# Performance work log

Hardware: AMD Instinct MI355X
Metric: run time of the kernel (lower is better)

The kernel has to match this reference:

```python
import jax, jax.numpy as jnp
import numpy as np

L, H, Z, B, SRC, K = 2, 1024, 256, 128, 64, 48
IN = Z + 1 + H  # z_i (+) k (+) attn


def _init(key, shape, fan_in):
    return jax.random.normal(key, shape, jnp.float32) / np.sqrt(fan_in)


def setup_inputs() -> dict:
    key = jax.random.key(0)
    ks = jax.random.split(key, 24)
    inp = {
        "h0": jax.random.normal(ks[0], (L, B, H), jnp.float32),
        "c0": jax.random.normal(ks[1], (L, B, H), jnp.float32),
        "context": jax.random.normal(ks[2], (B, SRC, H), jnp.float32),
        "z_0": jax.random.normal(ks[3], (B, Z), jnp.float32),
        "k": jax.random.randint(ks[4], (B, 1), 1, K + 1, jnp.int32),
        "eps": jax.random.normal(ks[5], (K, B, Z), jnp.float32),
        # StackedLSTM layer 0 (input IN) and layer 1 (input H)
        "W_ih0": _init(ks[6], (4 * H, IN), IN), "W_hh0": _init(ks[7], (4 * H, H), H),
        "b_ih0": jnp.zeros((4 * H,), jnp.float32), "b_hh0": jnp.zeros((4 * H,), jnp.float32),
        "W_ih1": _init(ks[8], (4 * H, H), H), "W_hh1": _init(ks[9], (4 * H, H), H),
        "b_ih1": jnp.zeros((4 * H,), jnp.float32), "b_hh1": jnp.zeros((4 * H,), jnp.float32),
        # GlobalAttentionLatent (Luong general)
        "attn_W_in": _init(ks[10], (H, H), H), "attn_W_out": _init(ks[11], (H, 2 * H), 2 * H),
        # GeneratorLatent
        "mu_W": _init(ks[12], (Z, H), H), "mu_b": jnp.zeros((Z,), jnp.float32),
        "sigma_W": _init(ks[13], (Z, H), H), "sigma_b": jnp.zeros((Z,), jnp.float32),
    }
    return inp


def _lstm_cell(x, h, c, W_ih, W_hh, b_ih, b_hh):
    gates = x @ W_ih.T + b_ih + h @ W_hh.T + b_hh
    i, f, g, o = jnp.split(gates, 4, axis=1)
    c_new = jax.nn.sigmoid(f) * c + jax.nn.sigmoid(i) * jnp.tanh(g)
    h_new = jax.nn.sigmoid(o) * jnp.tanh(c_new)
    return h_new, c_new


def _attend(q, context, W_in, W_out):
    # q: [B,H], context: [B,S,H] -> [B,H]
    scores = jnp.einsum('bsh,bh->bs', context, q @ W_in.T)
    align = jax.nn.softmax(scores, axis=1)
    weighted = jnp.einsum('bs,bsh->bh', align, context)
    return jnp.tanh(jnp.concatenate([weighted, q], axis=1) @ W_out.T)


def _forward(h0, c0, context, z_0, k, eps,
             W_ih0, W_hh0, b_ih0, b_hh0, W_ih1, W_hh1, b_ih1, b_hh1,
             attn_W_in, attn_W_out, mu_W, mu_b, sigma_W, sigma_b):
    k_max = eps.shape[0]
    k_f = k.astype(jnp.float32)  # [B,1]
    attn0 = _attend(c0[-1], context, attn_W_in, attn_W_out)

    def step(carry, inp):
        z_i, attn_o, h, c = carry
        i, eps_i = inp
        x = jnp.concatenate([z_i, k_f, attn_o], axis=1)  # [B, Z+1+H]
        h0n, c0n = _lstm_cell(x, h[0], c[0], W_ih0, W_hh0, b_ih0, b_hh0)
        h1n, c1n = _lstm_cell(h0n, h[1], c[1], W_ih1, W_hh1, b_ih1, b_hh1)
        h_new = jnp.stack([h0n, h1n])
        c_new = jnp.stack([c0n, c1n])
        frozen = (i >= k_f).astype(h_new.dtype)[None]  # [1,B,1]
        h_new = frozen * h + (1.0 - frozen) * h_new
        c_new = frozen * c + (1.0 - frozen) * c_new
        output = h1n  # rnn output before freezing, as in torch
        mu_i = output @ mu_W.T + mu_b
        sig_i = output @ sigma_W.T + sigma_b
        z_next = mu_i + jnp.exp(sig_i) * eps_i
        attn_new = _attend(output, context, attn_W_in, attn_W_out)
        return (z_next, attn_new, h_new, c_new), (z_next, mu_i, sig_i)

    steps = jnp.arange(k_max, dtype=jnp.float32)
    (_, _, h_f, c_f), (z, mu, sigma) = jax.lax.scan(
        step, (z_0, attn0, h0, c0), (steps, eps))
    valid = (steps[:, None] < k_f[:, 0][None, :])[:, :, None]  # [K,B,1]
    z = jnp.where(valid, z, 0.0)
    mu = jnp.where(valid, mu, 0.0)
    sigma = jnp.where(valid, sigma, 0.0)
    return (z.transpose(1, 0, 2), mu.transpose(1, 0, 2), sigma.transpose(1, 0, 2), h_f, c_f)


def reference(h0, c0, context, z_0, k, eps,
              W_ih0, W_hh0, b_ih0, b_hh0, W_ih1, W_hh1, b_ih1, b_hh1,
              attn_W_in, attn_W_out, mu_W, mu_b, sigma_W, sigma_b):
    return _forward(h0, c0, context, z_0, k, eps,
                    W_ih0, W_hh0, b_ih0, b_hh0, W_ih1, W_hh1, b_ih1, b_hh1,
                    attn_W_in, attn_W_out, mu_W, mu_b, sigma_W, sigma_b)
```

## Files before the change

kernel.cpp:

```cpp
#include <hip/hip_runtime.h>
#include <hip/hip_bf16.h>

#define L_ 2
#define H_ 1024
#define Z_ 256
#define B_ 128
#define SRC_ 64
#define K_ 48
#define BH_ (B_ * H_)
#define BZ_ (B_ * Z_)
#define BKZ_ ((size_t)B_ * K_ * Z_)
#define KA_ 2304
#define KB_ 2048

typedef unsigned short u16;
typedef __attribute__((ext_vector_type(8))) short short8;
typedef __attribute__((ext_vector_type(4))) float f32x4;

__device__ __align__(16) u16 g_Wc0[4096 * KA_];
__device__ __align__(16) u16 g_Wc1[4096 * KB_];
__device__ __align__(16) u16 g_Wmq[512 * 1024];
__device__ __align__(16) u16 g_Woutb[1024 * 2048];
__device__ __align__(16) u16 g_WinT[1024 * 1024];
__device__ __align__(16) u16 g_ctxb[8192 * 1024];
__device__ __align__(16) u16 g_ctxW[8192 * 1024];
__device__ __align__(16) u16 g_ctxWin[8192 * 1024];
__device__ __align__(16) u16 g_XA[2][B_ * KA_];
__device__ __align__(16) u16 g_XB[2][B_ * KB_];
__device__ __align__(16) u16 g_XC[B_ * H_];
__device__ float g_pb0[4096], g_pb1[4096], g_pbmq[512], g_wk0[4096];
__device__ float g_cs0[BH_], g_cs1[BH_], g_align[B_ * SRC_];
__device__ float g_cred[B_ * H_];
__device__ int g_perm[B_], g_inv[B_], g_kr[B_], g_Mact[K_];

__device__ __forceinline__ float sigm(float x) { return 1.0f / (1.0f + expf(-x)); }
__device__ __forceinline__ u16 f2b(float f) {
    union { float f; unsigned u; } x; x.f = f;
    unsigned r = x.u + 0x7fffu + ((x.u >> 16) & 1u);
    return (u16)(r >> 16);
}
__device__ __forceinline__ float b2f(u16 s) {
    union { unsigned u; float f; } x; x.u = ((unsigned)s) << 16;
    return x.f;
}

#define PREPALL_NBLK_ 22017
__global__ __launch_bounds__(256) void k_prepall(
        const float* __restrict__ Wih0, const float* __restrict__ Whh0,
        const float* __restrict__ bih0, const float* __restrict__ bhh0,
        const float* __restrict__ Wih1, const float* __restrict__ Whh1,
        const float* __restrict__ bih1, const float* __restrict__ bhh1,
        const float* __restrict__ muW, const float* __restrict__ mub,
        const float* __restrict__ sgW, const float* __restrict__ sgb,
        const float* __restrict__ Win, const float* __restrict__ Wout,
        const float* __restrict__ ctx, const int* __restrict__ kvec,
        float* __restrict__ out) {
    __shared__ float shf[32 * 33];
    const int bid = blockIdx.x, tid = threadIdx.x;
    if (bid < 4096) {
        int n = bid, h = n >> 2, g = n & 3, r = g * 1024 + h;
        u16* row = g_Wc0 + (size_t)n * KA_;
        for (int j = tid; j < KA_; j += 256) {
            float v = (j < 256) ? Wih0[(size_t)r * 1281 + j]
                    : (j < 1280) ? Wih0[(size_t)r * 1281 + j + 1]
                                 : Whh0[(size_t)r * 1024 + (j - 1280)];
            row[j] = f2b(v);
        }
        if (tid == 0) {
            g_wk0[n] = Wih0[(size_t)r * 1281 + 256];
            g_pb0[n] = bih0[r] + bhh0[r];
        }
    } else if (bid < 8192) {
        int n = bid - 4096, h = n >> 2, g = n & 3, r = g * 1024 + h;
        u16* row = g_Wc1 + (size_t)n * KB_;
        for (int j = tid; j < KB_; j += 256) {
            float v = (j < 1024) ? Wih1[(size_t)r * 1024 + j]
                                 : Whh1[(size_t)r * 1024 + (j - 1024)];
            row[j] = f2b(v);
        }
        if (tid == 0) g_pb1[n] = bih1[r] + bhh1[r];
    } else if (bid < 8704) {
        int n = bid - 8192, z = n >> 1, sel = n & 1;
        const float* src = sel ? sgW : muW;
        u16* row = g_Wmq + (size_t)n * 1024;
        for (int j = tid; j < 1024; j += 256) row[j] = f2b(src[(size_t)z * 1024 + j]);
        if (tid == 0) g_pbmq[n] = sel ? sgb[z] : mub[z];
    } else if (bid < 9728) {
        int loc = bid - 8704;
        int bx = (loc & 31) * 32, by = (loc >> 5) * 32;
        int tx = tid & 31, ty0 = tid >> 5;
        for (int it = 0; it < 4; ++it) {
            int ty = ty0 + it * 8;
            shf[ty * 33 + tx] = Win[(size_t)(by + ty) * 1024 + bx + tx];
        }
        __syncthreads();
        for (int it = 0; it < 4; ++it) {
            int ty = ty0 + it * 8;
            g_WinT[(size_t)(bx + ty) * 1024 + by + tx] = f2b(shf[tx * 33 + ty]);
        }
    } else if (bid == 9728) {
        int* ks = (int*)shf;
        if (tid < B_) ks[tid] = kvec[tid];
        __syncthreads();
        if (tid < B_) {
            int kb = ks[tid], rank = 0;
            for (int j = 0; j < B_; ++j) {
                int kj = ks[j];
                rank += (kj > kb) || (kj == kb && j < tid);
            }
            g_perm[rank] = tid; g_inv[tid] = rank; g_kr[rank] = kb;
        }
        if (tid < K_) {
            int c = 0;
            for (int j = 0; j < B_; ++j) c += (ks[j] > tid);
            g_Mact[tid] = c;
        }
    } else if (bid < 11777) {
        int loc = bid - 9729;
        const int n = 1024 * 2048;
        for (int i = loc * 256 + tid; i < n; i += 2048 * 256)
            g_Woutb[i] = f2b(Wout[i]);
    } else if (bid < 19969) {
        int loc = bid - 11777;
        const int n = 8192 * 1024;
        for (int i = loc * 256 + tid; i < n; i += 8192 * 256)
            g_ctxb[i] = f2b(ctx[i]);
    } else {
        int loc = bid - 19969;
        size_t n = 3 * BKZ_;
        for (size_t i = (size_t)loc * 256 + tid; i < n; i += (size_t)2048 * 256)
            out[i] = 0.f;
    }
}

template <int K>
__device__ __forceinline__ void mmq(const u16* __restrict__ A, int sA,
                                    const u16* __restrict__ W, int sW,
                                    int m0, int n0, int w, int lane, f32x4& acc) {
    constexpr int KQ = K / 4;
    const int quad = lane >> 4, l16 = lane & 15;
    const u16* pa = A + (size_t)(m0 + l16) * sA + w * KQ + quad * 8;
    const u16* pw = W + (size_t)(n0 + l16) * sW + w * KQ + quad * 8;
#pragma unroll 4
    for (int k0 = 0; k0 < KQ; k0 += 32) {
        short8 a = *(const short8*)(const void*)(pa + k0);
        short8 b = *(const short8*)(const void*)(pw + k0);
        acc = __builtin_amdgcn_mfma_f32_16x16x32_bf16(a, b, acc, 0, 0, 0);
    }
}

__device__ __forceinline__ void stage_q(float* sm, int w, int lane, const f32x4& acc) {
    int quad = lane >> 4, l16 = lane & 15;
#pragma unroll
    for (int r = 0; r < 4; ++r) sm[w * 272 + (quad * 4 + r) * 17 + l16] = acc[r];
}

template <int K>
__device__ __forceinline__ void mm32(const u16* __restrict__ A, int sA,
                                     const u16* __restrict__ W, int sW,
                                     int m0, int n0, int w, int lane, f32x4 acc[2][2]) {
    constexpr int KQ = K / 4;
    const int quad = lane >> 4, l16 = lane & 15;
    const u16* pa0 = A + (size_t)(m0 + l16) * sA + w * KQ + quad * 8;
    const u16* pa1 = pa0 + (size_t)16 * sA;
    const u16* pb0 = W + (size_t)(n0 + l16) * sW + w * KQ + quad * 8;
    const u16* pb1 = pb0 + (size_t)16 * sW;
#pragma unroll 4
    for (int k0 = 0; k0 < KQ; k0 += 32) {
        short8 a0 = *(const short8*)(const void*)(pa0 + k0);
        short8 a1 = *(const short8*)(const void*)(pa1 + k0);
        short8 b0 = *(const short8*)(const void*)(pb0 + k0);
        short8 b1 = *(const short8*)(const void*)(pb1 + k0);
        acc[0][0] = __builtin_amdgcn_mfma_f32_16x16x32_bf16(a0, b0, acc[0][0], 0, 0, 0);
        acc[0][1] = __builtin_amdgcn_mfma_f32_16x16x32_bf16(a0, b1, acc[0][1], 0, 0, 0);
        acc[1][0] = __builtin_amdgcn_mfma_f32_16x16x32_bf16(a1, b0, acc[1][0], 0, 0, 0);
        acc[1][1] = __builtin_amdgcn_mfma_f32_16x16x32_bf16(a1, b1, acc[1][1], 0, 0, 0);
    }
}

template <int LAYER>
__global__ __launch_bounds__(256) void k_lstm(int step) {
    constexpr int K = (LAYER == 0) ? KA_ : KB_;
    const int p = step & 1;
    const u16* A = (LAYER == 0) ? g_XA[p] : g_XB[p];
    const u16* W = (LAYER == 0) ? g_Wc0 : g_Wc1;
    const float* pb = (LAYER == 0) ? g_pb0 : g_pb1;
    float* cs = (LAYER == 0) ? g_cs0 : g_cs1;
    const u16* stOld = (LAYER == 0) ? (g_XA[p] + 1280) : (g_XB[p] + 1024);
    u16* stNew = (LAYER == 0) ? (g_XA[1 - p] + 1280) : (g_XB[1 - p] + 1024);
    u16* hout = (LAYER == 0) ? g_XB[p] : g_XC;
    const int hoStride = (LAYER == 0) ? KB_ : 1024;

    const int tid = threadIdx.x, w = tid >> 6, lane = tid & 63;
    const int xcd = blockIdx.x & 7, loc = blockIdx.x >> 3;
    const int mt = loc & 3, nl = loc >> 2;
    const int m0 = mt * 32;
    const int n0 = (xcd * 16 + nl) * 32;
    const int Mact = g_Mact[step];

    if (m0 >= Mact) {
        const int r = m0 + (tid & 31), hg = (n0 >> 2) + (tid >> 5);
        stNew[(size_t)r * K + hg] = stOld[(size_t)r * K + hg];
        return;
    }

    __shared__ float smf[4 * 32 * 33];
    f32x4 acc[2][2] = {};
    mm32<K>(A, K, W, K, m0, n0, w, lane, acc);
    const int quad = lane >> 4, l16 = lane & 15;
#pragma unroll
    for (int i = 0; i < 2; ++i)
#pragma unroll
        for (int j = 0; j < 2; ++j)
#pragma unroll
            for (int r = 0; r < 4; ++r)
                smf[(w * 32 + i * 16 + quad * 4 + r) * 33 + j * 16 + l16] = acc[i][j][r];
    __syncthreads();
    const int bl = tid & 31, hl = tid >> 5;
    const int r = m0 + bl;
    float g[4];
#pragma unroll
    for (int gg = 0; gg < 4; ++gg) {
        int c = hl * 4 + gg;
        float s = smf[bl * 33 + c] + smf[(32 + bl) * 33 + c] +
                  smf[(64 + bl) * 33 + c] + smf[(96 + bl) * 33 + c];
        g[gg] = s + pb[n0 + c];
    }
    const int kr = g_kr[r];
    if (LAYER == 0) {
        float kf = (float)kr;
#pragma unroll
        for (int gg = 0; gg < 4; ++gg) g[gg] += kf * g_wk0[n0 + hl * 4 + gg];
    }
    const int hg = (n0 >> 2) + hl;
    float cold = cs[r * 1024 + hg];
    float cn = sigm(g[1]) * cold + sigm(g[0]) * tanhf(g[2]);
    float hn = sigm(g[3]) * tanhf(cn);
    hout[(size_t)r * hoStride + hg] = f2b(hn);
    if (step < kr) {
        stNew[(size_t)r * K + hg] = f2b(hn);
        cs[r * 1024 + hg] = cn;
    } else {
        stNew[(size_t)r * K + hg] = stOld[(size_t)r * K + hg];
    }
}

__global__ __launch_bounds__(256) void k_mix(const float* __restrict__ eps,
                                             float* __restrict__ out, int step,
                                             int do_mu, int do_sc) {
    __shared__ float sm[1344];
    const int tid = threadIdx.x;
    const int Mact = g_Mact[step];
    if (blockIdx.x < 256) {
        if (!do_mu) return;
        const int w = tid >> 6, lane = tid & 63;
        const int xcd = blockIdx.x & 7, loc = blockIdx.x >> 3;
        const int mt = loc & 7, nl = loc >> 3;
        const int m0 = mt * 16;
        const int n0 = (xcd * 4 + nl) * 16;
        if (m0 >= Mact) return;
        f32x4 acc = {0.f, 0.f, 0.f, 0.f};
        mmq<1024>(g_XC, 1024, g_Wmq, 1024, m0, n0, w, lane, acc);
        stage_q(sm, w, lane, acc);
        __syncthreads();
        if (tid < 128) {
            int bl = tid & 15, zl = tid >> 4;
            int r = m0 + bl;
            int c0 = 2 * zl, c1 = 2 * zl + 1;
            float mu = sm[bl * 17 + c0] + sm[272 + bl * 17 + c0] +
                       sm[544 + bl * 17 + c0] + sm[816 + bl * 17 + c0] + g_pbmq[n0 + c0];
            float sg = sm[bl * 17 + c1] + sm[272 + bl * 17 + c1] +
                       sm[544 + bl * 17 + c1] + sm[816 + bl * 17 + c1] + g_pbmq[n0 + c1];
            int zg = (n0 >> 1) + zl;
            int b = g_perm[r];
            float e = eps[((size_t)step * B_ + b) * Z_ + zg];
            float zn = mu + expf(sg) * e;
            g_XA[(step + 1) & 1][(size_t)r * KA_ + zg] = f2b(zn);
            bool valid = step < g_kr[r];
            size_t o = ((size_t)b * K_ + step) * Z_ + zg;
            out[o] = valid ? zn : 0.f;
            out[BKZ_ + o] = valid ? mu : 0.f;
            out[2 * BKZ_ + o] = valid ? sg : 0.f;
        }
    } else if (blockIdx.x < 384) {
        if (!do_sc) return;
        const int r = blockIdx.x - 256;
        if (r >= Mact) return;
        float* qf = sm;
        float* parts = sm + 1024;
        for (int i = tid; i < 1024; i += 256) qf[i] = b2f(g_XC[r * 1024 + i]);
        __syncthreads();
        int s = tid >> 2, part = tid & 3;
        const int b = g_perm[r];
        const u16* row = g_ctxWin + ((size_t)(b * SRC_ + s)) * 1024 + part * 256;
        float pacc = 0.f;
        for (int j = 0; j < 256; j += 8) {
            short8 v = *(const short8*)(const void*)(row + j);
#pragma unroll
            for (int t = 0; t < 8; ++t) pacc += qf[part * 256 + j + t] * b2f(((u16*)&v)[t]);
        }
        parts[s * 4 + part] = pacc;
        __syncthreads();
        if (tid < 64) {
            float v = parts[tid * 4] + parts[tid * 4 + 1] + parts[tid * 4 + 2] + parts[tid * 4 + 3];
            float mx = v;
            for (int o = 32; o; o >>= 1) mx = fmaxf(mx, __shfl_xor(mx, o, 64));
            float e = expf(v - mx), sum = e;
            for (int o = 32; o; o >>= 1) sum += __shfl_xor(sum, o, 64);
            g_align[r * SRC_ + tid] = e / sum;
        }
    } else {
        if (!do_sc) return;
        const int w = tid >> 6, lane = tid & 63;
        const int t = blockIdx.x - 384;
        const int xcd = t & 7, loc = t >> 3;
        const int mt = loc & 7, nl = loc >> 3;
        const int m0 = mt * 16;
        const int n0 = (xcd * 8 + nl) * 16;
        if (m0 >= Mact) return;
        f32x4 acc = {0.f, 0.f, 0.f, 0.f};
        mmq<1024>(g_XC, 1024, g_Woutb + 1024, 2048, m0, n0, w, lane, acc);
        stage_q(sm, w, lane, acc);
        __syncthreads();
        int bl = tid >> 4, hc = tid & 15;
        float cred = sm[bl * 17 + hc] + sm[272 + bl * 17 + hc] +
                     sm[544 + bl * 17 + hc] + sm[816 + bl * 17 + hc];
        g_cred[(size_t)(m0 + bl) * 1024 + n0 + hc] = cred;
    }
}

__global__ __launch_bounds__(256) void k_contract(int dp, int step) {
    __shared__ float sm[16 * SRC_];
    const int tid = threadIdx.x;
    const int xcd = blockIdx.x & 7, loc = blockIdx.x >> 3;
    const int mt = loc & 7, nl = loc >> 3;
    const int m0 = mt * 16;
    const int n0 = (xcd * 8 + nl) * 16;
    if (m0 >= g_Mact[step]) return;
    for (int i = tid; i < 16 * SRC_; i += 256)
        sm[i] = g_align[(m0 + (i >> 6)) * SRC_ + (i & 63)];
    __syncthreads();
    int bl = tid >> 4, hc = tid & 15;
    int r = m0 + bl;
    const int b = g_perm[r];
    const u16* base = g_ctxW + ((size_t)b * SRC_) * 1024 + n0 + hc;
    float a = g_cred[(size_t)r * 1024 + n0 + hc];
#pragma unroll 8
    for (int s = 0; s < SRC_; ++s) a += sm[bl * 64 + s] * b2f(base[(size_t)s * 1024]);
    g_XA[dp][(size_t)r * KA_ + 256 + n0 + hc] = f2b(tanhf(a));
}

__global__ __launch_bounds__(256) void k_gemminit(const float* __restrict__ h0,
                                                  const float* __restrict__ c0,
                                                  const float* __restrict__ z0) {
    const int bid = blockIdx.x, tid = threadIdx.x;
    if (bid < 2048) {
        const int sel = bid & 1;
        const int vb = bid >> 1;
        const u16* W = sel ? g_WinT : g_Woutb;
        const int sW = sel ? 1024 : 2048;
        u16* Out = sel ? g_ctxWin : g_ctxW;
        const int w = tid >> 6, lane = tid & 63;
        const int quad = lane >> 4, l16 = lane & 15;
        const int xcd = vb & 7, loc = vb >> 3;
        const int n0 = (xcd * 2 + (loc & 1)) * 64;
        const int mb = (loc >> 1) * 128 + w * 32;
        f32x4 acc[2][4] = {};
        const u16* pa0 = g_ctxb + (size_t)(mb + l16) * 1024 + quad * 8;
        const u16* pa1 = pa0 + (size_t)16 * 1024;
        const u16* pw = W + (size_t)(n0 + l16) * sW + quad * 8;
#pragma unroll 2
        for (int k0 = 0; k0 < 1024; k0 += 32) {
            short8 a0 = *(const short8*)(const void*)(pa0 + k0);
            short8 a1 = *(const short8*)(const void*)(pa1 + k0);
#pragma unroll
            for (int j = 0; j < 4; ++j) {
                short8 b = *(const short8*)(const void*)(pw + (size_t)j * 16 * sW + k0);
                acc[0][j] = __builtin_amdgcn_mfma_f32_16x16x32_bf16(a0, b, acc[0][j], 0, 0, 0);
                acc[1][j] = __builtin_amdgcn_mfma_f32_16x16x32_bf16(a1, b, acc[1][j], 0, 0, 0);
            }
        }
#pragma unroll
        for (int i = 0; i < 2; ++i)
#pragma unroll
            for (int j = 0; j < 4; ++j)
#pragma unroll
                for (int r = 0; r < 4; ++r)
                    Out[(size_t)(mb + i * 16 + quad * 4 + r) * 1024 + n0 + j * 16 + l16] =
                        f2b(acc[i][j][r]);
    } else {
        int i = (bid - 2048) * 256 + tid;
        int b = i >> 10, h = i & 1023;
        int r = g_inv[b];
        g_XA[0][(size_t)r * KA_ + 1280 + h] = f2b(h0[i]);
        g_XB[0][(size_t)r * KB_ + 1024 + h] = f2b(h0[BH_ + i]);
        g_XC[r * 1024 + h] = f2b(c0[BH_ + i]);
        g_cs0[r * 1024 + h] = c0[i];
        g_cs1[r * 1024 + h] = c0[BH_ + i];
        if (i < BZ_) {
            int bb = i >> 8, z = i & 255;
            g_XA[0][(size_t)g_inv[bb] * KA_ + z] = f2b(z0[i]);
        }
    }
}

__global__ void k_final(float* __restrict__ out) {
    int i = blockIdx.x * 256 + threadIdx.x;
    int b = i >> 10, h = i & 1023;
    int r = g_inv[b];
    float* hf = out + (size_t)3 * BKZ_;
    float* cf = hf + 2 * BH_;
    hf[i] = b2f(g_XA[0][(size_t)r * KA_ + 1280 + h]);
    hf[BH_ + i] = b2f(g_XB[0][(size_t)r * KB_ + 1024 + h]);
    cf[i] = g_cs0[r * 1024 + h];
    cf[BH_ + i] = g_cs1[r * 1024 + h];
}

extern "C" void kernel_launch(void* const* d_in, const int* in_sizes, int n_in,
                              void* d_out, int out_size, void* d_ws, size_t ws_size,
                              hipStream_t stream) {
    (void)in_sizes; (void)n_in; (void)out_size; (void)d_ws; (void)ws_size;
    const float* h0 = (const float*)d_in[0];
    const float* c0 = (const float*)d_in[1];
    const float* ctx = (const float*)d_in[2];
    const float* z0 = (const float*)d_in[3];
    const int* kvec = (const int*)d_in[4];
    const float* eps = (const float*)d_in[5];
    const float* Wih0 = (const float*)d_in[6];
    const float* Whh0 = (const float*)d_in[7];
    const float* bih0 = (const float*)d_in[8];
    const float* bhh0 = (const float*)d_in[9];
    const float* Wih1 = (const float*)d_in[10];
    const float* Whh1 = (const float*)d_in[11];
    const float* bih1 = (const float*)d_in[12];
    const float* bhh1 = (const float*)d_in[13];
    const float* Win = (const float*)d_in[14];
    const float* Wout = (const float*)d_in[15];
    const float* muW = (const float*)d_in[16];
    const float* mub = (const float*)d_in[17];
    const float* sgW = (const float*)d_in[18];
    const float* sgb = (const float*)d_in[19];
    float* out = (float*)d_out;

    dim3 blk(256);
    k_prepall<<<PREPALL_NBLK_, blk, 0, stream>>>(
        Wih0, Whh0, bih0, bhh0, Wih1, Whh1, bih1, bhh1,
        muW, mub, sgW, sgb, Win, Wout, ctx, kvec, out);
    k_gemminit<<<2560, blk, 0, stream>>>(h0, c0, z0);

    k_mix<<<896, blk, 0, stream>>>(eps, out, 0, 0, 1);
    k_contract<<<512, blk, 0, stream>>>(0, 0);

    for (int i = 0; i < K_; ++i) {
        k_lstm<0><<<512, blk, 0, stream>>>(i);
        k_lstm<1><<<512, blk, 0, stream>>>(i);
        const int more = (i + 1 < K_) ? 1 : 0;
        k_mix<<<more ? 896 : 256, blk, 0, stream>>>(eps, out, i, 1, more);
        if (more) k_contract<<<512, blk, 0, stream>>>((i + 1) & 1, i);
    }
    k_final<<<BH_ / 256, blk, 0, stream>>>(out);
}
```

Before: 3.087 ms.

## Fuse attention contraction into mix kernel using atomic counter handoff

Removes the separate k_contract launch per step by having the Wout-projection blocks in k_mix spin-wait on a per-row-tile atomic counter set by the softmax blocks, then read alignment weights via LLC-coherent loads and finish the context contraction in place. This eliminates one kernel launch and the g_cred round trip per step, at the cost of intra-grid spin waiting that relies on producer blocks being scheduled. Separately, the init GEMM output is staged through LDS so global stores are 16-byte vectorized.

```diff
diff --git a/kernel.cpp b/kernel.cpp
--- a/kernel.cpp
+++ b/kernel.cpp
@@ -30,8 +30,8 @@
 __device__ __align__(16) u16 g_XC[B_ * H_];
 __device__ float g_pb0[4096], g_pb1[4096], g_pbmq[512], g_wk0[4096];
 __device__ float g_cs0[BH_], g_cs1[BH_], g_align[B_ * SRC_];
-__device__ float g_cred[B_ * H_];
 __device__ int g_perm[B_], g_inv[B_], g_kr[B_], g_Mact[K_];
+__device__ int g_scnt[K_ + 1][8];
 
 __device__ __forceinline__ float sigm(float x) { return 1.0f / (1.0f + expf(-x)); }
 __device__ __forceinline__ u16 f2b(float f) {
@@ -42,6 +42,22 @@
 __device__ __forceinline__ float b2f(u16 s) {
     union { unsigned u; float f; } x; x.u = ((unsigned)s) << 16;
     return x.f;
+}
+
+__device__ __forceinline__ void st32_llc(float* p, float v) {
+    asm volatile("global_store_dword %0, %1, off sc0 sc1" :: "v"(p), "v"(v) : "memory");
+}
+__device__ __forceinline__ unsigned ld32u_llc(const unsigned* p) {
+    unsigned r;
+    asm volatile("global_load_dword %0, %1, off sc0 sc1\n\ts_waitcnt vmcnt(0)"
+                 : "=v"(r) : "v"(p) : "memory");
+    return r;
+}
+__device__ __forceinline__ f32x4 ld128f_llc(const float* p) {
+    f32x4 r;
+    asm volatile("global_load_dwordx4 %0, %1, off sc0 sc1\n\ts_waitcnt vmcnt(0)"
+                 : "=v"(r) : "v"(p) : "memory");
+    return r;
 }
 
 #define PREPALL_NBLK_ 22017
@@ -115,6 +131,7 @@
             for (int j = 0; j < B_; ++j) c += (ks[j] > tid);
             g_Mact[tid] = c;
         }
+        for (int i = tid; i < (K_ + 1) * 8; i += 256) ((int*)g_scnt)[i] = 0;
     } else if (bid < 11777) {
         int loc = bid - 9729;
         const int n = 1024 * 2048;
@@ -246,9 +263,9 @@
 }
 
 __global__ __launch_bounds__(256) void k_mix(const float* __restrict__ eps,
-                                             float* __restrict__ out, int step,
-                                             int do_mu, int do_sc) {
-    __shared__ float sm[1344];
+                                             float* __restrict__ out, int step, int dp,
+                                             int cidx, int do_mu, int do_sc) {
+    __shared__ float sm[2112];
     const int tid = threadIdx.x;
     const int Mact = g_Mact[step];
     if (blockIdx.x < 256) {
@@ -275,7 +292,7 @@
             int b = g_perm[r];
             float e = eps[((size_t)step * B_ + b) * Z_ + zg];
             float zn = mu + expf(sg) * e;
-            g_XA[(step + 1) & 1][(size_t)r * KA_ + zg] = f2b(zn);
+            g_XA[dp][(size_t)r * KA_ + zg] = f2b(zn);
             bool valid = step < g_kr[r];
             size_t o = ((size_t)b * K_ + step) * Z_ + zg;
             out[o] = valid ? zn : 0.f;
@@ -307,8 +324,12 @@
             for (int o = 32; o; o >>= 1) mx = fmaxf(mx, __shfl_xor(mx, o, 64));
             float e = expf(v - mx), sum = e;
             for (int o = 32; o; o >>= 1) sum += __shfl_xor(sum, o, 64);
-            g_align[r * SRC_ + tid] = e / sum;
-        }
+            st32_llc(&g_align[r * SRC_ + tid], e / sum);
+        }
+        asm volatile("s_waitcnt vmcnt(0)" ::: "memory");
+        if (tid == 0)
+            __hip_atomic_fetch_add(&g_scnt[cidx][r >> 4], 1,
+                                   __ATOMIC_RELAXED, __HIP_MEMORY_SCOPE_AGENT);
     } else {
         if (!do_sc) return;
         const int w = tid >> 6, lane = tid & 63;
@@ -322,37 +343,36 @@
         mmq<1024>(g_XC, 1024, g_Woutb + 1024, 2048, m0, n0, w, lane, acc);
         stage_q(sm, w, lane, acc);
         __syncthreads();
-        int bl = tid >> 4, hc = tid & 15;
+        const int bl = tid >> 4, hc = tid & 15;
         float cred = sm[bl * 17 + hc] + sm[272 + bl * 17 + hc] +
                      sm[544 + bl * 17 + hc] + sm[816 + bl * 17 + hc];
-        g_cred[(size_t)(m0 + bl) * 1024 + n0 + hc] = cred;
-    }
-}
-
-__global__ __launch_bounds__(256) void k_contract(int dp, int step) {
-    __shared__ float sm[16 * SRC_];
-    const int tid = threadIdx.x;
-    const int xcd = blockIdx.x & 7, loc = blockIdx.x >> 3;
-    const int mt = loc & 7, nl = loc >> 3;
-    const int m0 = mt * 16;
-    const int n0 = (xcd * 8 + nl) * 16;
-    if (m0 >= g_Mact[step]) return;
-    for (int i = tid; i < 16 * SRC_; i += 256)
-        sm[i] = g_align[(m0 + (i >> 6)) * SRC_ + (i & 63)];
-    __syncthreads();
-    int bl = tid >> 4, hc = tid & 15;
-    int r = m0 + bl;
-    const int b = g_perm[r];
-    const u16* base = g_ctxW + ((size_t)b * SRC_) * 1024 + n0 + hc;
-    float a = g_cred[(size_t)r * 1024 + n0 + hc];
+        const int act = (Mact - m0 < 16) ? (Mact - m0) : 16;
+        if (tid == 0) {
+            while ((int)ld32u_llc((const unsigned*)&g_scnt[cidx][mt]) < act)
+                __builtin_amdgcn_s_sleep(2);
+        }
+        __syncthreads();
+        float* al = sm + 1088;
+        {
+            f32x4 v = ld128f_llc(g_align + (size_t)m0 * SRC_ + tid * 4);
+            al[tid * 4 + 0] = v[0]; al[tid * 4 + 1] = v[1];
+            al[tid * 4 + 2] = v[2]; al[tid * 4 + 3] = v[3];
+        }
+        __syncthreads();
+        const int r = m0 + bl;
+        const int b = g_perm[r];
+        const u16* base = g_ctxW + ((size_t)b * SRC_) * 1024 + n0 + hc;
+        float a = cred;
 #pragma unroll 8
-    for (int s = 0; s < SRC_; ++s) a += sm[bl * 64 + s] * b2f(base[(size_t)s * 1024]);
-    g_XA[dp][(size_t)r * KA_ + 256 + n0 + hc] = f2b(tanhf(a));
+        for (int s = 0; s < SRC_; ++s) a += al[bl * 64 + s] * b2f(base[(size_t)s * 1024]);
+        g_XA[dp][(size_t)r * KA_ + 256 + n0 + hc] = f2b(tanhf(a));
+    }
 }
 
 __global__ __launch_bounds__(256) void k_gemminit(const float* __restrict__ h0,
                                                   const float* __restrict__ c0,
                                                   const float* __restrict__ z0) {
+    __shared__ u16 st[4][32][72];
     const int bid = blockIdx.x, tid = threadIdx.x;
     if (bid < 2048) {
         const int sel = bid & 1;
@@ -380,14 +400,21 @@
                 acc[1][j] = __builtin_amdgcn_mfma_f32_16x16x32_bf16(a1, b, acc[1][j], 0, 0, 0);
             }
         }
+        u16 (*my)[72] = st[w];
 #pragma unroll
         for (int i = 0; i < 2; ++i)
 #pragma unroll
             for (int j = 0; j < 4; ++j)
 #pragma unroll
                 for (int r = 0; r < 4; ++r)
-                    Out[(size_t)(mb + i * 16 + quad * 4 + r) * 1024 + n0 + j * 16 + l16] =
-                        f2b(acc[i][j][r]);
+                    my[i * 16 + quad * 4 + r][j * 16 + l16] = f2b(acc[i][j][r]);
+#pragma unroll
+        for (int it = 0; it < 4; ++it) {
+            int idx = it * 64 + lane;
+            int row = idx >> 3, seg = idx & 7;
+            short8 v = *(const short8*)(const void*)&my[row][seg * 8];
+            *(short8*)(void*)(Out + (size_t)(mb + row) * 1024 + n0 + seg * 8) = v;
+        }
     } else {
         int i = (bid - 2048) * 256 + tid;
         int b = i >> 10, h = i & 1023;
@@ -448,15 +475,13 @@
         muW, mub, sgW, sgb, Win, Wout, ctx, kvec, out);
     k_gemminit<<<2560, blk, 0, stream>>>(h0, c0, z0);
 
-    k_mix<<<896, blk, 0, stream>>>(eps, out, 0, 0, 1);
-    k_contract<<<512, blk, 0, stream>>>(0, 0);
+    k_mix<<<896, blk, 0, stream>>>(eps, out, 0, 0, 0, 0, 1);
 
     for (int i = 0; i < K_; ++i) {
         k_lstm<0><<<512, blk, 0, stream>>>(i);
         k_lstm<1><<<512, blk, 0, stream>>>(i);
         const int more = (i + 1 < K_) ? 1 : 0;
-        k_mix<<<more ? 896 : 256, blk, 0, stream>>>(eps, out, i, 1, more);
-        if (more) k_contract<<<512, blk, 0, stream>>>((i + 1) & 1, i);
+        k_mix<<<more ? 896 : 256, blk, 0, stream>>>(eps, out, i, (i + 1) & 1, i + 1, 1, more);
     }
     k_final<<<BH_ / 256, blk, 0, stream>>>(out);
 }
```

Result: slower. 3.216 ms (+4.2%).
